# Kernel tuning notes

Measured on AMD Instinct MI355X. Metric: run time of the kernel, lower is better.

The kernel has to match this reference:

```python
import jax, jax.numpy as jnp
import numpy as np

B, N, C, W = 64, 4096, 128, 64
WIN = N - W + 1  # 4033, length of each sliding-filter input
BN_EPS = 1e-5


def setup_inputs() -> dict:
    key = jax.random.key(0)
    ks = jax.random.split(key, 8)
    s_in = 1.0 / np.sqrt(WIN)   # nn.Linear default init scale
    s_2 = 1.0 / np.sqrt(2.0)
    s_out = 1.0 / np.sqrt(W)
    return {
        "x": jax.random.normal(ks[0], (B, N, C, 2), dtype=jnp.float32),
        "w_in_real": jax.random.normal(ks[1], (C, WIN), dtype=jnp.float32) * s_in,
        "w_in_imag": jax.random.normal(ks[2], (C, WIN), dtype=jnp.float32) * s_in,
        "A_nonlin": jax.random.normal(ks[3], (C, 2, 2), dtype=jnp.float32) * s_2,
        "Wc": jax.random.normal(ks[4], (2, 2), dtype=jnp.float32) * s_2,
        "w_out_real": jax.random.normal(ks[5], (C, W), dtype=jnp.float32) * s_out,
        "w_out_imag": jax.random.normal(ks[6], (C, W), dtype=jnp.float32) * s_out,
        "bn_gamma": jnp.ones((C,), dtype=jnp.float32),
        "bn_beta": jnp.zeros((C,), dtype=jnp.float32),
    }


def _depthwise_corr(sig, w):
    # sig: [B, N, C], w: [C, K] -> [B, N-K+1, C]
    # filtered[b, t, c] = sum_k sig[b, t+k, c] * w[c, k]  (matches per-channel Linear on slices)
    rhs = w.T[:, None, :]  # [K, 1, C]
    return jax.lax.conv_general_dilated(
        sig, rhs, window_strides=(1,), padding="VALID",
        dimension_numbers=("NWC", "WIO", "NWC"),
        feature_group_count=sig.shape[-1])


def reference(x, w_in_real, w_in_imag, A_nonlin, Wc, w_out_real, w_out_imag, bn_gamma, bn_beta):
    xr, xi = x[..., 0], x[..., 1]               # [B, N, C]
    # --- per-channel sliding input filters (out_window positions) ---
    fr = _depthwise_corr(xr, w_in_real)          # [B, W, C]
    fi = _depthwise_corr(xi, w_in_imag)          # [B, W, C]
    v = jnp.stack([fr, fi], axis=-1)             # [B, W, C, 2]
    # --- per-channel 2x2 linear: out_j = sum_i A[c, j, i] * v_i ---
    u = jnp.einsum("bwci,cji->bwcj", v, A_nonlin)
    amp = jnp.sum(u * u, axis=-1, keepdims=True)  # r^2 + i^2
    u = amp * u
    # --- shared 2x2 coeff linear ---
    u = jnp.einsum("bwci,ji->bwcj", u, Wc)
    # --- per-channel output filters over the out_window axis ---
    out_r = jnp.einsum("bwc,cw->bc", u[..., 0], w_out_real)
    out_i = jnp.einsum("bwc,cw->bc", u[..., 1], w_out_imag)
    out = jnp.stack([out_r, out_i], axis=-1)     # [B, C, 2]
    # --- BatchNorm1d(C), training-mode batch statistics over (B, last) dims ---
    mean = jnp.mean(out, axis=(0, 2), keepdims=True)
    var = jnp.mean((out - mean) ** 2, axis=(0, 2), keepdims=True)
    out = (out - mean) * jax.lax.rsqrt(var + BN_EPS)
    return out * bn_gamma[None, :, None] + bn_beta[None, :, None]
```

## Files before the change

kernel.cpp:

```cpp
#include <hip/hip_runtime.h>

typedef float v2f __attribute__((ext_vector_type(2)));

#define B_ 64
#define N_ 4096
#define C_ 128
#define W_ 64
#define WIN_ 4033
#define CG 16
#define NCHUNK 128
#define NSPLIT 2
#define KPAD 4176
#define WROW 192
#define WSTRIDE 193

__global__ void prep_w(const float* __restrict__ wr, const float* __restrict__ wi,
                       v2f* __restrict__ w2pad) {
  int idx = blockIdx.x * 256 + threadIdx.x;
  int c = idx / KPAD;
  int kk = idx - c * KPAD;
  int k = kk - 64;
  v2f v = {0.f, 0.f};
  if (k >= 0 && k < WIN_) {
    v.x = wr[c * WIN_ + k];
    v.y = wi[c * WIN_ + k];
  }
  w2pad[idx] = v;
}

__global__ __launch_bounds__(256, 3) void conv_main(
    const v2f* __restrict__ x2,
    const v2f* __restrict__ w2pad,
    v2f* __restrict__ fq) {
  __shared__ __attribute__((aligned(16))) v2f wsh[CG * WSTRIDE];

  int tid = threadIdx.x;
  int bid = blockIdx.x;
  int cg = bid & 7;
  int bb = (bid >> 3) & 63;
  int ns = bid >> 9;
  int cbase = cg * CG;
  int cl = tid & 15;
  int t0g = (tid >> 4) & 3;
  int np = tid >> 6;
  int t0 = t0g << 4;
  int nbase = np << 5;

  v2f zero = {0.f, 0.f};
  v2f acc[16];
#pragma unroll
  for (int i = 0; i < 16; i++) acc[i] = zero;

  const v2f* xg = x2 + (size_t)bb * N_ * C_ + cbase + cl;
  const v2f* wrow = wsh + cl * WSTRIDE;

  int nstart = ns * (N_ / NSPLIT);
  int nend = nstart + N_ / NSPLIT;

  auto do16 = [&](int nb, const v2f* xv, const v2f* wold, v2f* wnew) {
#pragma unroll
    for (int j = 0; j < 16; j++) wnew[j] = wrow[nb + 64 - t0 + j];
#pragma unroll
    for (int j = 0; j < 16; j++) {
#pragma unroll
      for (int i = 0; i < 16; i++) {
        int e = j - i;
        v2f wv = (e < 0) ? wold[16 + e] : wnew[e];
        acc[i] = __builtin_elementwise_fma(xv[j], wv, acc[i]);
      }
    }
  };

  for (int n0 = nstart; n0 < nend; n0 += NCHUNK) {
    {
      const v2f* wsrc = w2pad + (size_t)cbase * KPAD + n0;
#pragma unroll
      for (int k = 0; k < 12; k++) {
        int i = tid + k * 256;
        int c = i / WROW;
        int u = i - c * WROW;
        wsh[c * WSTRIDE + u] = wsrc[(size_t)c * KPAD + u];
      }
    }
    __syncthreads();

    v2f wA[16], wB[16], xA[16], xB[16];
#pragma unroll
    for (int m = 0; m < 16; m++) wA[m] = wrow[nbase + 48 - t0 + m];
#pragma unroll
    for (int j = 0; j < 16; j++) xA[j] = xg[(size_t)(n0 + nbase + j) * C_];
#pragma unroll
    for (int j = 0; j < 16; j++) xB[j] = xg[(size_t)(n0 + nbase + 16 + j) * C_];

    do16(nbase + 0, xA, wA, wB);
    do16(nbase + 16, xB, wB, wA);
    __syncthreads();
  }

  v2f* fpart = wsh;
  if (np >= 2) {
#pragma unroll
    for (int i = 0; i < 16; i++) fpart[(np - 2) * 1040 + cl * 65 + t0 + i] = acc[i];
  }
  __syncthreads();
  if (np < 2) {
#pragma unroll
    for (int i = 0; i < 16; i++) acc[i] += fpart[np * 1040 + cl * 65 + t0 + i];
  }
  __syncthreads();
  if (np == 1) {
#pragma unroll
    for (int i = 0; i < 16; i++) fpart[cl * 65 + t0 + i] = acc[i];
  }
  __syncthreads();
  if (np == 0) {
    v2f* out = fq + (size_t)(ns * B_ + bb) * 64 * C_ + cbase + cl;
#pragma unroll
    for (int i = 0; i < 16; i++) {
      v2f r = acc[i] + fpart[cl * 65 + t0 + i];
      out[(size_t)(t0 + i) * C_] = r;
    }
  }
}

__global__ void nonlin_out(const v2f* __restrict__ fq, const float* __restrict__ Anl,
                           const float* __restrict__ Wcm, const float* __restrict__ wor,
                           const float* __restrict__ woi, v2f* __restrict__ pre) {
  int b = blockIdx.x;
  int c = threadIdx.x;
  float a00 = Anl[c * 4 + 0], a01 = Anl[c * 4 + 1];
  float a10 = Anl[c * 4 + 2], a11 = Anl[c * 4 + 3];
  float wc00 = Wcm[0], wc01 = Wcm[1], wc10 = Wcm[2], wc11 = Wcm[3];
  const v2f* f0 = fq + (size_t)b * 64 * C_ + c;
  const v2f* f1 = fq + (size_t)(B_ + b) * 64 * C_ + c;
  float or_ = 0.f, oi_ = 0.f;
#pragma unroll 4
  for (int t = 0; t < 64; t++) {
    v2f f = f0[(size_t)t * C_] + f1[(size_t)t * C_];
    float ur = a00 * f.x + a01 * f.y;
    float ui = a10 * f.x + a11 * f.y;
    float amp = ur * ur + ui * ui;
    ur *= amp;
    ui *= amp;
    float vr = wc00 * ur + wc01 * ui;
    float vi = wc10 * ur + wc11 * ui;
    or_ += vr * wor[c * 64 + t];
    oi_ += vi * woi[c * 64 + t];
  }
  v2f r = {or_, oi_};
  pre[(size_t)b * C_ + c] = r;
}

__global__ void bn_kernel(const float* __restrict__ pre, const float* __restrict__ gamma,
                          const float* __restrict__ beta, float* __restrict__ out) {
  int c = blockIdx.x, tid = threadIdx.x;
  int b = tid >> 1, comp = tid & 1;
  float v = pre[((size_t)b * C_ + c) * 2 + comp];
  float s = v, s2 = v * v;
#pragma unroll
  for (int d = 32; d > 0; d >>= 1) {
    s += __shfl_down(s, d, 64);
    s2 += __shfl_down(s2, d, 64);
  }
  __shared__ float red[4];
  if ((tid & 63) == 0) {
    red[(tid >> 6) * 2 + 0] = s;
    red[(tid >> 6) * 2 + 1] = s2;
  }
  __syncthreads();
  float sum = red[0] + red[2], sumsq = red[1] + red[3];
  float mean = sum * 0.0078125f;
  float var = sumsq * 0.0078125f - mean * mean;
  float inv = rsqrtf(var + 1e-5f);
  out[((size_t)b * C_ + c) * 2 + comp] = (v - mean) * inv * gamma[c] + beta[c];
}

extern "C" void kernel_launch(void* const* d_in, const int* in_sizes, int n_in,
                              void* d_out, int out_size, void* d_ws, size_t ws_size,
                              hipStream_t stream) {
  (void)in_sizes; (void)n_in; (void)out_size; (void)ws_size;
  const float* x   = (const float*)d_in[0];
  const float* wir = (const float*)d_in[1];
  const float* wii = (const float*)d_in[2];
  const float* Anl = (const float*)d_in[3];
  const float* Wcm = (const float*)d_in[4];
  const float* wrr = (const float*)d_in[5];
  const float* wri = (const float*)d_in[6];
  const float* gam = (const float*)d_in[7];
  const float* bet = (const float*)d_in[8];

  v2f* w2pad = (v2f*)d_ws;
  v2f* fq = (v2f*)((char*)d_ws + (size_t)C_ * KPAD * sizeof(v2f));
  v2f* pre = (v2f*)((char*)fq + (size_t)NSPLIT * B_ * 64 * C_ * sizeof(v2f));

  prep_w<<<(C_ * KPAD) / 256, 256, 0, stream>>>(wir, wii, w2pad);
  conv_main<<<B_ * 8 * NSPLIT, 256, 0, stream>>>((const v2f*)x, w2pad, fq);
  nonlin_out<<<B_, C_, 0, stream>>>(fq, Anl, Wcm, wrr, wri, pre);
  bn_kernel<<<C_, 128, 0, stream>>>((const float*)pre, gam, bet, (float*)d_out);
}
```

Baseline: 468.0 us.

## Double-buffer conv weights via direct global-to-LDS loads and prefetch x chunks

The conv kernel now stages filter weights into two LDS buffers using global_load_lds, so the next chunk's weights are fetched while the current chunk computes. Input x registers are also prefetched one chunk ahead, and the chunk size is halved to 64. This is meant to hide global-memory latency behind the FMA loop, at the cost of more LDS, more registers and more barriers per unit of work. The nonlin_out kernel is also split across 256 threads, with a shared-memory reduction combining the two halves of the time axis.

```diff
diff --git a/kernel.cpp b/kernel.cpp
--- a/kernel.cpp
+++ b/kernel.cpp
@@ -8,11 +8,12 @@
 #define W_ 64
 #define WIN_ 4033
 #define CG 16
-#define NCHUNK 128
+#define NCHUNK 64
 #define NSPLIT 2
 #define KPAD 4176
-#define WROW 192
-#define WSTRIDE 193
+#define WROW 128
+#define WSTRIDE 130
+#define LDSBUF (CG * WSTRIDE)
 
 __global__ void prep_w(const float* __restrict__ wr, const float* __restrict__ wi,
                        v2f* __restrict__ w2pad) {
@@ -32,7 +33,7 @@
     const v2f* __restrict__ x2,
     const v2f* __restrict__ w2pad,
     v2f* __restrict__ fq) {
-  __shared__ __attribute__((aligned(16))) v2f wsh[CG * WSTRIDE];
+  __shared__ __attribute__((aligned(16))) v2f wsh[2 * LDSBUF];
 
   int tid = threadIdx.x;
   int bid = blockIdx.x;
@@ -41,10 +42,11 @@
   int ns = bid >> 9;
   int cbase = cg * CG;
   int cl = tid & 15;
-  int t0g = (tid >> 4) & 3;
+  int t0 = ((tid >> 4) & 3) << 4;
   int np = tid >> 6;
-  int t0 = t0g << 4;
-  int nbase = np << 5;
+  int nbase = np << 4;
+  int lane = tid & 63;
+  int wv_ = tid >> 6;
 
   v2f zero = {0.f, 0.f};
   v2f acc[16];
@@ -52,49 +54,63 @@
   for (int i = 0; i < 16; i++) acc[i] = zero;
 
   const v2f* xg = x2 + (size_t)bb * N_ * C_ + cbase + cl;
-  const v2f* wrow = wsh + cl * WSTRIDE;
-
   int nstart = ns * (N_ / NSPLIT);
-  int nend = nstart + N_ / NSPLIT;
-
-  auto do16 = [&](int nb, const v2f* xv, const v2f* wold, v2f* wnew) {
-#pragma unroll
-    for (int j = 0; j < 16; j++) wnew[j] = wrow[nb + 64 - t0 + j];
+
+  auto stage = [&](int buf, int n0s) {
+#pragma unroll
+    for (int rr = 0; rr < 4; rr++) {
+      int r = wv_ * 4 + rr;
+      const char* src =
+          (const char*)(w2pad + (size_t)(cbase + r) * KPAD + n0s) + (size_t)lane * 16;
+      v2f* dst = wsh + buf * LDSBUF + r * WSTRIDE;
+      __builtin_amdgcn_global_load_lds(
+          (const __attribute__((address_space(1))) unsigned int*)src,
+          (__attribute__((address_space(3))) unsigned int*)dst, 16, 0, 0);
+    }
+  };
+
+  auto loadx = [&](int n0x, v2f* xv) {
+#pragma unroll
+    for (int j = 0; j < 16; j++) xv[j] = xg[(size_t)(n0x + nbase + j) * C_];
+  };
+
+  auto chunk = [&](int buf, const v2f* xC, v2f* xN, int sn0, int xn0) {
+    stage(buf ^ 1, sn0);
+    const v2f* wrow = wsh + buf * LDSBUF + cl * WSTRIDE;
+    v2f wA[16], wB[16];
+#pragma unroll
+    for (int m = 0; m < 16; m++) wA[m] = wrow[nbase + 48 - t0 + m];
+    loadx(xn0, xN);
+#pragma unroll
+    for (int j = 0; j < 16; j++) wB[j] = wrow[nbase + 64 - t0 + j];
 #pragma unroll
     for (int j = 0; j < 16; j++) {
 #pragma unroll
       for (int i = 0; i < 16; i++) {
         int e = j - i;
-        v2f wv = (e < 0) ? wold[16 + e] : wnew[e];
-        acc[i] = __builtin_elementwise_fma(xv[j], wv, acc[i]);
-      }
-    }
-  };
-
-  for (int n0 = nstart; n0 < nend; n0 += NCHUNK) {
-    {
-      const v2f* wsrc = w2pad + (size_t)cbase * KPAD + n0;
-#pragma unroll
-      for (int k = 0; k < 12; k++) {
-        int i = tid + k * 256;
-        int c = i / WROW;
-        int u = i - c * WROW;
-        wsh[c * WSTRIDE + u] = wsrc[(size_t)c * KPAD + u];
+        v2f wvv = (e < 0) ? wA[16 + e] : wB[e];
+        acc[i] = __builtin_elementwise_fma(xC[j], wvv, acc[i]);
       }
     }
     __syncthreads();
-
-    v2f wA[16], wB[16], xA[16], xB[16];
-#pragma unroll
-    for (int m = 0; m < 16; m++) wA[m] = wrow[nbase + 48 - t0 + m];
-#pragma unroll
-    for (int j = 0; j < 16; j++) xA[j] = xg[(size_t)(n0 + nbase + j) * C_];
-#pragma unroll
-    for (int j = 0; j < 16; j++) xB[j] = xg[(size_t)(n0 + nbase + 16 + j) * C_];
-
-    do16(nbase + 0, xA, wA, wB);
-    do16(nbase + 16, xB, wB, wA);
-    __syncthreads();
+  };
+
+  v2f xE[16], xO[16];
+  stage(0, nstart);
+  loadx(nstart, xE);
+  __syncthreads();
+
+  const int WLIM = KPAD - WROW;
+  const int XLIM = N_ - NCHUNK;
+
+  for (int k = 0; k < (N_ / NSPLIT) / NCHUNK; k += 2) {
+    int n0 = nstart + k * NCHUNK;
+    int s1 = n0 + NCHUNK;
+    chunk(0, xE, xO, s1, s1);
+    int s2 = n0 + 2 * NCHUNK;
+    int s2w = s2 > WLIM ? WLIM : s2;
+    int s2x = s2 > XLIM ? XLIM : s2;
+    chunk(1, xO, xE, s2w, s2x);
   }
 
   v2f* fpart = wsh;
@@ -127,15 +143,17 @@
                            const float* __restrict__ Wcm, const float* __restrict__ wor,
                            const float* __restrict__ woi, v2f* __restrict__ pre) {
   int b = blockIdx.x;
-  int c = threadIdx.x;
+  int tid = threadIdx.x;
+  int c = tid & 127, th = tid >> 7;
   float a00 = Anl[c * 4 + 0], a01 = Anl[c * 4 + 1];
   float a10 = Anl[c * 4 + 2], a11 = Anl[c * 4 + 3];
   float wc00 = Wcm[0], wc01 = Wcm[1], wc10 = Wcm[2], wc11 = Wcm[3];
   const v2f* f0 = fq + (size_t)b * 64 * C_ + c;
   const v2f* f1 = fq + (size_t)(B_ + b) * 64 * C_ + c;
   float or_ = 0.f, oi_ = 0.f;
-#pragma unroll 4
-  for (int t = 0; t < 64; t++) {
+#pragma unroll 8
+  for (int tt = 0; tt < 32; tt++) {
+    int t = th * 32 + tt;
     v2f f = f0[(size_t)t * C_] + f1[(size_t)t * C_];
     float ur = a00 * f.x + a01 * f.y;
     float ui = a10 * f.x + a11 * f.y;
@@ -147,8 +165,16 @@
     or_ += vr * wor[c * 64 + t];
     oi_ += vi * woi[c * 64 + t];
   }
-  v2f r = {or_, oi_};
-  pre[(size_t)b * C_ + c] = r;
+  __shared__ float redr[128], redi[128];
+  if (th == 1) {
+    redr[c] = or_;
+    redi[c] = oi_;
+  }
+  __syncthreads();
+  if (th == 0) {
+    v2f r = {or_ + redr[c], oi_ + redi[c]};
+    pre[(size_t)b * C_ + c] = r;
+  }
 }
 
 __global__ void bn_kernel(const float* __restrict__ pre, const float* __restrict__ gamma,
@@ -195,6 +221,6 @@
 
   prep_w<<<(C_ * KPAD) / 256, 256, 0, stream>>>(wir, wii, w2pad);
   conv_main<<<B_ * 8 * NSPLIT, 256, 0, stream>>>((const v2f*)x, w2pad, fq);
-  nonlin_out<<<B_, C_, 0, stream>>>(fq, Anl, Wcm, wrr, wri, pre);
+  nonlin_out<<<B_, 256, 0, stream>>>(fq, Anl, Wcm, wrr, wri, pre);
   bn_kernel<<<C_, 128, 0, stream>>>((const float*)pre, gam, bet, (float*)d_out);
 }
```

Result: no change. 470.3 us (+0.5%).

## Split conv N-range four ways with atomic accumulation and raise occupancy

Applied to the files above, without the earlier changes.

The sequence dimension of the depthwise conv is now split into four blocks per (batch, channel group) instead of two, doubling the grid to expose more parallelism. Partial sums are combined with float atomicAdd into a single zero-initialized buffer, which needs a new zero_fq kernel. The launch-bounds occupancy hint rises from 3 to 6 blocks, which may force register spilling given the 16-element v2f accumulator and the buffered x and w registers. The nonlinearity kernel now splits the time loop across two thread halves and reduces through shared memory. Float atomics also make the summation order nondeterministic.

```diff
diff --git a/kernel.cpp b/kernel.cpp
--- a/kernel.cpp
+++ b/kernel.cpp
@@ -1,6 +1,7 @@
 #include <hip/hip_runtime.h>
 
 typedef float v2f __attribute__((ext_vector_type(2)));
+typedef float v4f __attribute__((ext_vector_type(4)));
 
 #define B_ 64
 #define N_ 4096
@@ -9,7 +10,7 @@
 #define WIN_ 4033
 #define CG 16
 #define NCHUNK 128
-#define NSPLIT 2
+#define NSPLIT 4
 #define KPAD 4176
 #define WROW 192
 #define WSTRIDE 193
@@ -28,7 +29,11 @@
   w2pad[idx] = v;
 }
 
-__global__ __launch_bounds__(256, 3) void conv_main(
+__global__ void zero_fq(v4f* __restrict__ fqv) {
+  fqv[(size_t)blockIdx.x * 256 + threadIdx.x] = (v4f){0.f, 0.f, 0.f, 0.f};
+}
+
+__global__ __launch_bounds__(256, 6) void conv_main(
     const v2f* __restrict__ x2,
     const v2f* __restrict__ w2pad,
     v2f* __restrict__ fq) {
@@ -41,9 +46,8 @@
   int ns = bid >> 9;
   int cbase = cg * CG;
   int cl = tid & 15;
-  int t0g = (tid >> 4) & 3;
+  int t0 = ((tid >> 4) & 3) << 4;
   int np = tid >> 6;
-  int t0 = t0g << 4;
   int nbase = np << 5;
 
   v2f zero = {0.f, 0.f};
@@ -71,6 +75,7 @@
     }
   };
 
+#pragma unroll 1
   for (int n0 = nstart; n0 < nend; n0 += NCHUNK) {
     {
       const v2f* wsrc = w2pad + (size_t)cbase * KPAD + n0;
@@ -114,11 +119,13 @@
   }
   __syncthreads();
   if (np == 0) {
-    v2f* out = fq + (size_t)(ns * B_ + bb) * 64 * C_ + cbase + cl;
+    float* op = (float*)(fq + (size_t)bb * 64 * C_ + cbase + cl);
 #pragma unroll
     for (int i = 0; i < 16; i++) {
       v2f r = acc[i] + fpart[cl * 65 + t0 + i];
-      out[(size_t)(t0 + i) * C_] = r;
+      size_t off = (size_t)(t0 + i) * C_ * 2;
+      atomicAdd(op + off + 0, r.x);
+      atomicAdd(op + off + 1, r.y);
     }
   }
 }
@@ -127,16 +134,17 @@
                            const float* __restrict__ Wcm, const float* __restrict__ wor,
                            const float* __restrict__ woi, v2f* __restrict__ pre) {
   int b = blockIdx.x;
-  int c = threadIdx.x;
+  int tid = threadIdx.x;
+  int c = tid & 127, th = tid >> 7;
   float a00 = Anl[c * 4 + 0], a01 = Anl[c * 4 + 1];
   float a10 = Anl[c * 4 + 2], a11 = Anl[c * 4 + 3];
   float wc00 = Wcm[0], wc01 = Wcm[1], wc10 = Wcm[2], wc11 = Wcm[3];
   const v2f* f0 = fq + (size_t)b * 64 * C_ + c;
-  const v2f* f1 = fq + (size_t)(B_ + b) * 64 * C_ + c;
   float or_ = 0.f, oi_ = 0.f;
-#pragma unroll 4
-  for (int t = 0; t < 64; t++) {
-    v2f f = f0[(size_t)t * C_] + f1[(size_t)t * C_];
+#pragma unroll 8
+  for (int tt = 0; tt < 32; tt++) {
+    int t = th * 32 + tt;
+    v2f f = f0[(size_t)t * C_];
     float ur = a00 * f.x + a01 * f.y;
     float ui = a10 * f.x + a11 * f.y;
     float amp = ur * ur + ui * ui;
@@ -147,8 +155,16 @@
     or_ += vr * wor[c * 64 + t];
     oi_ += vi * woi[c * 64 + t];
   }
-  v2f r = {or_, oi_};
-  pre[(size_t)b * C_ + c] = r;
+  __shared__ float redr[128], redi[128];
+  if (th == 1) {
+    redr[c] = or_;
+    redi[c] = oi_;
+  }
+  __syncthreads();
+  if (th == 0) {
+    v2f r = {or_ + redr[c], oi_ + redi[c]};
+    pre[(size_t)b * C_ + c] = r;
+  }
 }
 
 __global__ void bn_kernel(const float* __restrict__ pre, const float* __restrict__ gamma,
@@ -191,10 +207,11 @@
 
   v2f* w2pad = (v2f*)d_ws;
   v2f* fq = (v2f*)((char*)d_ws + (size_t)C_ * KPAD * sizeof(v2f));
-  v2f* pre = (v2f*)((char*)fq + (size_t)NSPLIT * B_ * 64 * C_ * sizeof(v2f));
+  v2f* pre = (v2f*)((char*)fq + (size_t)B_ * 64 * C_ * sizeof(v2f));
 
   prep_w<<<(C_ * KPAD) / 256, 256, 0, stream>>>(wir, wii, w2pad);
+  zero_fq<<<1024, 256, 0, stream>>>((v4f*)fq);
   conv_main<<<B_ * 8 * NSPLIT, 256, 0, stream>>>((const v2f*)x, w2pad, fq);
-  nonlin_out<<<B_, C_, 0, stream>>>(fq, Anl, Wcm, wrr, wri, pre);
+  nonlin_out<<<B_, 256, 0, stream>>>(fq, Anl, Wcm, wrr, wri, pre);
   bn_kernel<<<C_, 128, 0, stream>>>((const float*)pre, gam, bet, (float*)d_out);
 }
```

Result: slower. 795.0 us (+69.9%).
